# Optimization experiments

Hardware: AMD Instinct MI355X
Metric: run time of the kernel (lower is better)

The kernel has to match this reference:

```python
import jax, jax.numpy as jnp
import numpy as np

EPS = 1e-6
N_HEADS = 8


def causal_dot_product(q, k, v):
    # q,k: [n,h,l,d]; v: [n,h,l,m]
    kv = jnp.einsum('nhld,nhlm->nhldm', k, v)          # [n,h,l,d,m] (large, matches original)
    kv = jnp.cumsum(kv, axis=2)
    return jnp.einsum('nhld,nhldm->nhlm', q, kv)


def flow_attention_causal(queries, keys, values, Wq, bq, Wk, bk, Wv, bv, Wo, bo):
    B, L, _ = queries.shape
    H = N_HEADS
    # projections + split heads -> [B,H,L,Dh]
    def proj(x, W, b):
        y = x @ W + b
        return y.reshape(B, L, H, -1).transpose(0, 2, 1, 3)
    q = jax.nn.sigmoid(proj(queries, Wq, bq))
    k = jax.nn.sigmoid(proj(keys, Wk, bk))
    v = proj(values, Wv, bv)

    normal = (jnp.arange(L, dtype=q.dtype) + 1.0)[None, None, :]  # [1,1,L]

    sink_incoming = 1.0 / jnp.einsum('nhld,nhld->nhl', q + EPS, jnp.cumsum(k, axis=2) + EPS)
    source_outgoing = 1.0 / jnp.einsum('nhld,nhld->nhl', k + EPS, jnp.cumsum(q, axis=2) + EPS)
    sink_incoming = sink_incoming * normal
    source_outgoing = source_outgoing * normal

    conserved_sink = jnp.einsum('nhld,nhld->nhl', q + EPS,
                                jnp.cumsum(k * source_outgoing[..., None], axis=2) + EPS) / normal
    conserved_source = jnp.einsum('nhld,nhld->nhl', k + EPS,
                                  jnp.cumsum(q * sink_incoming[..., None], axis=2) + EPS) / normal
    conserved_source = jnp.clip(conserved_source, -1.0, 1.0)

    sink_allocation = jax.nn.sigmoid(conserved_sink)
    conserved_source = jnp.exp(conserved_source)
    source_competition = conserved_source / jnp.cumsum(conserved_source, axis=-1) * normal

    x = causal_dot_product(q * (sink_incoming / normal)[..., None],
                           k,
                           v * source_competition[..., None]) * sink_allocation[..., None]
    x = x.transpose(0, 2, 1, 3).reshape(B, L, -1)
    return x @ Wo + bo  # dropout is identity at eval


def setup_inputs() -> dict:
    key = jax.random.key(0)
    ks = jax.random.split(key, 11)
    B, L, Din, Dm, Dout = 2, 1024, 512, 512, 512
    s = 0.02
    return {
        'queries': jax.random.normal(ks[0], (B, L, Din), jnp.float32),
        'keys': jax.random.normal(ks[1], (B, L, Din), jnp.float32),
        'values': jax.random.normal(ks[2], (B, L, Din), jnp.float32),
        'Wq': jax.random.normal(ks[3], (Din, Dm), jnp.float32) * s,
        'bq': jnp.zeros((Dm,), jnp.float32),
        'Wk': jax.random.normal(ks[4], (Din, Dm), jnp.float32) * s,
        'bk': jnp.zeros((Dm,), jnp.float32),
        'Wv': jax.random.normal(ks[5], (Din, Dm), jnp.float32) * s,
        'bv': jnp.zeros((Dm,), jnp.float32),
        'Wo': jax.random.normal(ks[6], (Dm, Dout), jnp.float32) * s,
        'bo': jnp.zeros((Dout,), jnp.float32),
    }


def reference(queries, keys, values, Wq, bq, Wk, bk, Wv, bv, Wo, bo):
    return flow_attention_causal(queries, keys, values, Wq, bq, Wk, bk, Wv, bv, Wo, bo)
```

## Files before the change

kernel.cpp:

```cpp
#include <hip/hip_runtime.h>
#include <math.h>

#define EPSF 1e-6f

constexpr int B_  = 2;
constexpr int L_  = 1024;
constexpr int D_  = 512;
constexpr int H_  = 8;
constexpr int DH_ = 64;
constexpr int BL_ = B_ * L_;
constexpr int BH_ = B_ * H_;
constexpr int CT_ = 64;
constexpr int NC_ = L_ / CT_;

typedef __attribute__((ext_vector_type(8))) short bf16x8;
typedef __attribute__((ext_vector_type(4))) float f32x4;

__device__ __forceinline__ unsigned short f2bf(float f) {
  union { float f; unsigned int u; } v; v.f = f;
  const unsigned int u = v.u;
  return (unsigned short)((u + 0x7FFFu + ((u >> 16) & 1u)) >> 16);
}
__device__ __forceinline__ float bf2f(unsigned short u) {
  union { unsigned int u; float f; } v; v.u = ((unsigned int)u) << 16;
  return v.f;
}

__device__ __forceinline__ int sw(int row, int col) {
  return row * 64 + (col ^ ((row & 7) << 3));
}

__global__ __launch_bounds__(256) void proj3_k(const float* __restrict__ Qin,
                                               const float* __restrict__ Kin,
                                               const float* __restrict__ Vin,
                                               const float* __restrict__ Wq,
                                               const float* __restrict__ bq,
                                               const float* __restrict__ Wk,
                                               const float* __restrict__ bk,
                                               const float* __restrict__ Wv,
                                               const float* __restrict__ bv,
                                               unsigned short* __restrict__ Qb,
                                               unsigned short* __restrict__ Kb,
                                               unsigned short* __restrict__ Vb,
                                               float* __restrict__ sumQ,
                                               float* __restrict__ sumK) {
  const int z = blockIdx.z;
  const float* A    = (z == 0) ? Qin : (z == 1) ? Kin : Vin;
  const float* W    = (z == 0) ? Wq  : (z == 1) ? Wk  : Wv;
  const float* bias = (z == 0) ? bq  : (z == 1) ? bk  : bv;
  unsigned short* out = (z == 0) ? Qb : (z == 1) ? Kb : Vb;
  float* csum       = (z == 0) ? sumQ : (z == 1) ? sumK : nullptr;
  const bool sig = (z < 2);

  __shared__ __align__(16) short Als[64 * 40];
  __shared__ __align__(16) short Bls[64 * 40];
  const int tid = threadIdx.x;
  const int m0 = blockIdx.x * 64, n0 = blockIdx.y * 64;
  const int arow = tid >> 2, akq = (tid & 3) << 3;
  const int bcol = tid & 63, bk0 = (tid >> 6) << 3;
  const int lane = tid & 63, wid = tid >> 6;
  const int wr = wid >> 1, wc = wid & 1;
  const int lrow = lane & 15, lk = (lane >> 4) << 3;

  f32x4 acc[2][2] = {{{0.f, 0.f, 0.f, 0.f}, {0.f, 0.f, 0.f, 0.f}},
                     {{0.f, 0.f, 0.f, 0.f}, {0.f, 0.f, 0.f, 0.f}}};
  float ra[8], rb[8];

  auto loadAB = [&](int kt) {
    const float4 f0 = *(const float4*)&A[(size_t)(m0 + arow) * D_ + kt + akq];
    const float4 f1 = *(const float4*)&A[(size_t)(m0 + arow) * D_ + kt + akq + 4];
    ra[0] = f0.x; ra[1] = f0.y; ra[2] = f0.z; ra[3] = f0.w;
    ra[4] = f1.x; ra[5] = f1.y; ra[6] = f1.z; ra[7] = f1.w;
    const float* gw = &W[(size_t)(kt + bk0) * D_ + n0 + bcol];
#pragma unroll
    for (int j = 0; j < 8; ++j) rb[j] = gw[(size_t)j * D_];
  };
  auto writeLDS = [&]() {
    bf16x8 pa, pb;
#pragma unroll
    for (int j = 0; j < 8; ++j) {
      pa[j] = (short)f2bf(ra[j]);
      pb[j] = (short)f2bf(rb[j]);
    }
    *(bf16x8*)&Als[arow * 40 + akq] = pa;
    *(bf16x8*)&Bls[bcol * 40 + bk0] = pb;
  };
  auto compute = [&]() {
    bf16x8 a0 = *(const bf16x8*)&Als[(wr * 32 + lrow) * 40 + lk];
    bf16x8 a1 = *(const bf16x8*)&Als[(wr * 32 + 16 + lrow) * 40 + lk];
    bf16x8 b0 = *(const bf16x8*)&Bls[(wc * 32 + lrow) * 40 + lk];
    bf16x8 b1 = *(const bf16x8*)&Bls[(wc * 32 + 16 + lrow) * 40 + lk];
    acc[0][0] = __builtin_amdgcn_mfma_f32_16x16x32_bf16(a0, b0, acc[0][0], 0, 0, 0);
    acc[0][1] = __builtin_amdgcn_mfma_f32_16x16x32_bf16(a0, b1, acc[0][1], 0, 0, 0);
    acc[1][0] = __builtin_amdgcn_mfma_f32_16x16x32_bf16(a1, b0, acc[1][0], 0, 0, 0);
    acc[1][1] = __builtin_amdgcn_mfma_f32_16x16x32_bf16(a1, b1, acc[1][1], 0, 0, 0);
  };

  loadAB(0);
  writeLDS();
  for (int kt = 32; kt < D_; kt += 32) {
    loadAB(kt);
    __syncthreads();
    compute();
    __syncthreads();
    writeLDS();
  }
  __syncthreads();
  compute();

  const int b = m0 >> 10, h = n0 >> 6;
  float psum[2] = {0.f, 0.f};
#pragma unroll
  for (int j = 0; j < 2; ++j) {
    const int col = n0 + wc * 32 + j * 16 + lrow;
    const float bv4 = bias[col];
    const int dh = col & 63;
#pragma unroll
    for (int i = 0; i < 2; ++i) {
#pragma unroll
      for (int r = 0; r < 4; ++r) {
        const int row = m0 + wr * 32 + i * 16 + (lane >> 4) * 4 + r;
        float x = acc[i][j][r] + bv4;
        if (sig) x = 1.0f / (1.0f + expf(-x));
        const unsigned short ub = f2bf(x);
        const int l = row & (L_ - 1);
        out[(((size_t)(b * H_ + h)) * L_ + l) * DH_ + dh] = ub;
        psum[j] += bf2f(ub);
      }
    }
  }
  if (csum) {
    float* sumS = (float*)Als;
#pragma unroll
    for (int j = 0; j < 2; ++j) {
      psum[j] += __shfl_xor(psum[j], 16);
      psum[j] += __shfl_xor(psum[j], 32);
      if ((lane >> 4) == 0) sumS[wr * 64 + wc * 32 + j * 16 + lrow] = psum[j];
    }
    __syncthreads();
    if (tid < 64) {
      const int c = (m0 & (L_ - 1)) >> 6;
      const int bc = (b * H_ + h) * NC_ + c;
      csum[bc * DH_ + tid] = sumS[tid] + sumS[64 + tid];
    }
  }
}

__global__ __launch_bounds__(256) void flow_phase1_k(const unsigned short* __restrict__ Qb,
                                                     const unsigned short* __restrict__ Kb,
                                                     const float* __restrict__ sumQ,
                                                     const float* __restrict__ sumK,
                                                     float* __restrict__ qscale,
                                                     float* __restrict__ si_a,
                                                     float* __restrict__ so_a,
                                                     float* __restrict__ sumQSI,
                                                     float* __restrict__ sumKSO) {
  const int bc = blockIdx.x, bh = bc >> 4, c = bc & (NC_ - 1);
  const int g = bc * CT_;
  const int tid = threadIdx.x, lane = tid & 63, w = tid >> 6;
  __shared__ float qS[64][65], kS[64][65];
  __shared__ float pqS[64], pkS[64];
  __shared__ float aS[4][64], bS[4][64];
  __shared__ float siS[64], soS[64];
#pragma unroll
  for (int it = 0; it < 2; ++it) {
    const int i8 = it * 256 + tid;
    const int row = i8 >> 3, d0 = (i8 & 7) << 3;
    const bf16x8 qv = *(const bf16x8*)&Qb[(size_t)g * DH_ + i8 * 8];
    const bf16x8 kv = *(const bf16x8*)&Kb[(size_t)g * DH_ + i8 * 8];
#pragma unroll
    for (int j = 0; j < 8; ++j) {
      qS[row][d0 + j] = bf2f((unsigned short)qv[j]);
      kS[row][d0 + j] = bf2f((unsigned short)kv[j]);
    }
  }
  if (tid < 64) {
    float pq = 0.f, pk = 0.f;
    for (int cc = 0; cc < c; ++cc) {
      pq += sumQ[(bh * NC_ + cc) * DH_ + tid];
      pk += sumK[(bh * NC_ + cc) * DH_ + tid];
    }
    pqS[tid] = pq; pkS[tid] = pk;
  }
  __syncthreads();
  float ap = 0.f, bp = 0.f;
  for (int dd = 0; dd < 16; ++dd) {
    const int d = w * 16 + dd;
    const float qv = qS[lane][d];
    const float kv = kS[lane][d];
    float ck = kv, cq = qv;
#pragma unroll
    for (int off = 1; off < 64; off <<= 1) {
      const float t1 = __shfl_up(ck, off);
      const float t2 = __shfl_up(cq, off);
      ck += (lane >= off) ? t1 : 0.f;
      cq += (lane >= off) ? t2 : 0.f;
    }
    ck += pkS[d];
    cq += pqS[d];
    ap += (qv + EPSF) * (ck + EPSF);
    bp += (kv + EPSF) * (cq + EPSF);
  }
  aS[w][lane] = ap; bS[w][lane] = bp;
  __syncthreads();
  const float normal = (float)(c * CT_ + lane + 1);
  if (w == 0) {
    const float a = aS[0][lane] + aS[1][lane] + aS[2][lane] + aS[3][lane];
    const float b = bS[0][lane] + bS[1][lane] + bS[2][lane] + bS[3][lane];
    const float si = normal / a, so = normal / b;
    qscale[g + lane] = 1.0f / a;
    si_a[g + lane] = si;
    so_a[g + lane] = so;
    siS[lane] = si; soS[lane] = so;
  }
  __syncthreads();
  float sq = 0.f, sk = 0.f;
#pragma unroll
  for (int li = 0; li < 16; ++li) {
    const int l = w * 16 + li;
    sq += qS[l][lane] * siS[l];
    sk += kS[l][lane] * soS[l];
  }
  aS[w][lane] = sq; bS[w][lane] = sk;
  __syncthreads();
  if (tid < 64) {
    sumQSI[bc * DH_ + tid] = aS[0][tid] + aS[1][tid] + aS[2][tid] + aS[3][tid];
    sumKSO[bc * DH_ + tid] = bS[0][tid] + bS[1][tid] + bS[2][tid] + bS[3][tid];
  }
}

__global__ __launch_bounds__(256) void flow_phase2_k(const unsigned short* __restrict__ Qb,
                                                     const unsigned short* __restrict__ Kb,
                                                     const float* __restrict__ sumQSI,
                                                     const float* __restrict__ sumKSO,
                                                     const float* __restrict__ si_a,
                                                     const float* __restrict__ so_a,
                                                     float* __restrict__ salloc,
                                                     float* __restrict__ e_a,
                                                     float* __restrict__ sumE) {
  const int bc = blockIdx.x, bh = bc >> 4, c = bc & (NC_ - 1);
  const int g = bc * CT_;
  const int tid = threadIdx.x, lane = tid & 63, w = tid >> 6;
  __shared__ float qS[64][65], kS[64][65];
  __shared__ float pqS[64], pkS[64];
  __shared__ float aS[4][64], bS[4][64];
#pragma unroll
  for (int it = 0; it < 2; ++it) {
    const int i8 = it * 256 + tid;
    const int row = i8 >> 3, d0 = (i8 & 7) << 3;
    const bf16x8 qv = *(const bf16x8*)&Qb[(size_t)g * DH_ + i8 * 8];
    const bf16x8 kv = *(const bf16x8*)&Kb[(size_t)g * DH_ + i8 * 8];
#pragma unroll
    for (int j = 0; j < 8; ++j) {
      qS[row][d0 + j] = bf2f((unsigned short)qv[j]);
      kS[row][d0 + j] = bf2f((unsigned short)kv[j]);
    }
  }
  if (tid < 64) {
    float pq = 0.f, pk = 0.f;
    for (int cc = 0; cc < c; ++cc) {
      pq += sumQSI[(bh * NC_ + cc) * DH_ + tid];
      pk += sumKSO[(bh * NC_ + cc) * DH_ + tid];
    }
    pqS[tid] = pq; pkS[tid] = pk;
  }
  __syncthreads();
  const float si = si_a[g + lane];
  const float so = so_a[g + lane];
  float c1p = 0.f, c2p = 0.f;
  for (int dd = 0; dd < 16; ++dd) {
    const int d = w * 16 + dd;
    const float qv = qS[lane][d];
    const float kv = kS[lane][d];
    float ckso = kv * so, cqsi = qv * si;
#pragma unroll
    for (int off = 1; off < 64; off <<= 1) {
      const float t1 = __shfl_up(ckso, off);
      const float t2 = __shfl_up(cqsi, off);
      ckso += (lane >= off) ? t1 : 0.f;
      cqsi += (lane >= off) ? t2 : 0.f;
    }
    ckso += pkS[d];
    cqsi += pqS[d];
    c1p += (qv + EPSF) * (ckso + EPSF);
    c2p += (kv + EPSF) * (cqsi + EPSF);
  }
  aS[w][lane] = c1p; bS[w][lane] = c2p;
  __syncthreads();
  if (w == 0) {
    const float c1 = aS[0][lane] + aS[1][lane] + aS[2][lane] + aS[3][lane];
    const float c2 = bS[0][lane] + bS[1][lane] + bS[2][lane] + bS[3][lane];
    const float normal = (float)(c * CT_ + lane + 1);
    const float cs_sink = c1 / normal;
    salloc[g + lane] = 1.0f / (1.0f + expf(-cs_sink));
    float cs_src = c2 / normal;
    cs_src = fminf(1.0f, fmaxf(-1.0f, cs_src));
    const float e = expf(cs_src);
    e_a[g + lane] = e;
    float tot = e;
#pragma unroll
    for (int off = 32; off; off >>= 1) tot += __shfl_xor(tot, off);
    if (lane == 0) sumE[bc] = tot;
  }
}

__global__ __launch_bounds__(256) void flow_ckv_k(const unsigned short* __restrict__ K16,
                                                  const unsigned short* __restrict__ V16,
                                                  const float* __restrict__ e_a,
                                                  const float* __restrict__ sumE,
                                                  float* __restrict__ comp,
                                                  float* __restrict__ KV) {
  const int bc = blockIdx.x, bh = bc >> 4, c = bc & (NC_ - 1);
  const int g = bc * CT_;
  const int tid = threadIdx.x;
  __shared__ float compS[CT_];
  __shared__ __align__(16) unsigned short kT16[64 * 64];
  __shared__ __align__(16) unsigned short vT16[64 * 64];
  if (tid < 64) {
    const int lane = tid;
    const float e = e_a[g + lane];
    float se = (lane < c) ? sumE[bh * NC_ + lane] : 0.f;
#pragma unroll
    for (int off = 32; off; off >>= 1) se += __shfl_xor(se, off);
    float s = e;
#pragma unroll
    for (int off = 1; off < 64; off <<= 1) {
      const float t = __shfl_up(s, off);
      s += (lane >= off) ? t : 0.f;
    }
    const float cf = e / (se + s) * (float)(c * CT_ + lane + 1);
    compS[lane] = cf;
    comp[g + lane] = cf;
  }
  __syncthreads();
#pragma unroll
  for (int it = 0; it < 2; ++it) {
    const int i8 = it * 256 + tid;
    const int l = i8 >> 3, d0 = (i8 & 7) << 3;
    const bf16x8 kv = *(const bf16x8*)&K16[(size_t)g * DH_ + i8 * 8];
    const bf16x8 vv = *(const bf16x8*)&V16[(size_t)g * DH_ + i8 * 8];
    const float cl = compS[l];
#pragma unroll
    for (int j = 0; j < 8; ++j) {
      kT16[sw(d0 + j, l)] = (unsigned short)kv[j];
      vT16[sw(d0 + j, l)] = f2bf(bf2f((unsigned short)vv[j]) * cl);
    }
  }
  __syncthreads();
  const int lane = tid & 63, w = tid >> 6;
  const int fr = lane & 15, fk = (lane >> 4) << 3;
  f32x4 acc[4] = {{0.f, 0.f, 0.f, 0.f}, {0.f, 0.f, 0.f, 0.f},
                  {0.f, 0.f, 0.f, 0.f}, {0.f, 0.f, 0.f, 0.f}};
  const bf16x8 a0 = *(const bf16x8*)&kT16[sw(w * 16 + fr, fk)];
  const bf16x8 a1 = *(const bf16x8*)&kT16[sw(w * 16 + fr, fk + 32)];
#pragma unroll
  for (int cb = 0; cb < 4; ++cb) {
    const bf16x8 b0 = *(const bf16x8*)&vT16[sw(cb * 16 + fr, fk)];
    const bf16x8 b1 = *(const bf16x8*)&vT16[sw(cb * 16 + fr, fk + 32)];
    acc[cb] = __builtin_amdgcn_mfma_f32_16x16x32_bf16(a0, b0, acc[cb], 0, 0, 0);
    acc[cb] = __builtin_amdgcn_mfma_f32_16x16x32_bf16(a1, b1, acc[cb], 0, 0, 0);
  }
  float* outp = KV + (size_t)bc * DH_ * DH_;
#pragma unroll
  for (int r = 0; r < 4; ++r) {
    const int d = w * 16 + (lane >> 4) * 4 + r;
#pragma unroll
    for (int cb = 0; cb < 4; ++cb) outp[d * DH_ + cb * 16 + fr] = acc[cb][r];
  }
}

__global__ __launch_bounds__(256) void kv_prefix_k(float* __restrict__ KV) {
  const int idx = blockIdx.x * 256 + threadIdx.x;
  const int bh = idx >> 12, p = idx & 4095;
  const size_t base = (size_t)bh * NC_ * DH_ * DH_ + p;
  float run = 0.f;
#pragma unroll
  for (int c = 0; c < NC_; ++c) {
    const float t = KV[base + (size_t)c * DH_ * DH_];
    KV[base + (size_t)c * DH_ * DH_] = run;
    run += t;
  }
}

__global__ __launch_bounds__(256) void attn_k(const unsigned short* __restrict__ Q16,
                                              const unsigned short* __restrict__ K16,
                                              const unsigned short* __restrict__ V16,
                                              const float* __restrict__ KVp,
                                              const float* __restrict__ qscale,
                                              const float* __restrict__ salloc,
                                              const float* __restrict__ comp,
                                              unsigned short* __restrict__ X) {
  const int bc = blockIdx.x;
  const int bh = bc >> 4, c = bc & (NC_ - 1);
  const int bb = bh >> 3, hh = bh & (H_ - 1);
  const int g = bc * CT_;
  __shared__ __align__(16) unsigned short qp16[64 * 64];
  __shared__ __align__(16) unsigned short k16[64 * 64];
  __shared__ __align__(16) unsigned short vT16[64 * 64];
  __shared__ __align__(16) unsigned short kvT16[64 * 64];
  __shared__ __align__(16) unsigned short S16[64 * 64];
  const int tid = threadIdx.x;
#pragma unroll
  for (int it = 0; it < 2; ++it) {
    const int i8 = it * 256 + tid;
    const int r = i8 >> 3, d0 = (i8 & 7) << 3;
    const bf16x8 qv = *(const bf16x8*)&Q16[(size_t)g * DH_ + i8 * 8];
    const bf16x8 kv = *(const bf16x8*)&K16[(size_t)g * DH_ + i8 * 8];
    const bf16x8 vv = *(const bf16x8*)&V16[(size_t)g * DH_ + i8 * 8];
    const float qs = qscale[g + r];
    const float cl = comp[g + r];
    bf16x8 pq;
#pragma unroll
    for (int j = 0; j < 8; ++j) pq[j] = (short)f2bf(bf2f((unsigned short)qv[j]) * qs);
    *(bf16x8*)&qp16[sw(r, d0)] = pq;
    *(bf16x8*)&k16[sw(r, d0)] = kv;
#pragma unroll
    for (int j = 0; j < 8; ++j)
      vT16[sw(d0 + j, r)] = f2bf(bf2f((unsigned short)vv[j]) * cl);
  }
  for (int i4 = tid; i4 < DH_ * DH_ / 4; i4 += 256) {
    const int d = i4 >> 4, m0 = (i4 & 15) << 2;
    const float4 t = *(const float4*)&KVp[(size_t)bc * DH_ * DH_ + d * DH_ + m0];
    kvT16[sw(m0 + 0, d)] = f2bf(t.x);
    kvT16[sw(m0 + 1, d)] = f2bf(t.y);
    kvT16[sw(m0 + 2, d)] = f2bf(t.z);
    kvT16[sw(m0 + 3, d)] = f2bf(t.w);
  }
  __syncthreads();

  const int lane = tid & 63, w = tid >> 6;
  const int fr = lane & 15, fk = (lane >> 4) << 3;
  const int arow = w * 16 + fr;
  f32x4 accX[4] = {{0.f, 0.f, 0.f, 0.f}, {0.f, 0.f, 0.f, 0.f},
                   {0.f, 0.f, 0.f, 0.f}, {0.f, 0.f, 0.f, 0.f}};
  f32x4 accS[4] = {{0.f, 0.f, 0.f, 0.f}, {0.f, 0.f, 0.f, 0.f},
                   {0.f, 0.f, 0.f, 0.f}, {0.f, 0.f, 0.f, 0.f}};

  const bf16x8 aq0 = *(const bf16x8*)&qp16[sw(arow, fk)];
  const bf16x8 aq1 = *(const bf16x8*)&qp16[sw(arow, fk + 32)];
#pragma unroll
  for (int cb = 0; cb < 4; ++cb) {
    const int bcol = cb * 16 + fr;
    const bf16x8 bv0 = *(const bf16x8*)&kvT16[sw(bcol, fk)];
    const bf16x8 bv1 = *(const bf16x8*)&kvT16[sw(bcol, fk + 32)];
    accX[cb] = __builtin_amdgcn_mfma_f32_16x16x32_bf16(aq0, bv0, accX[cb], 0, 0, 0);
    accX[cb] = __builtin_amdgcn_mfma_f32_16x16x32_bf16(aq1, bv1, accX[cb], 0, 0, 0);
    const bf16x8 bk0 = *(const bf16x8*)&k16[sw(bcol, fk)];
    const bf16x8 bk1 = *(const bf16x8*)&k16[sw(bcol, fk + 32)];
    accS[cb] = __builtin_amdgcn_mfma_f32_16x16x32_bf16(aq0, bk0, accS[cb], 0, 0, 0);
    accS[cb] = __builtin_amdgcn_mfma_f32_16x16x32_bf16(aq1, bk1, accS[cb], 0, 0, 0);
  }
#pragma unroll
  for (int cb = 0; cb < 4; ++cb) {
#pragma unroll
    for (int r = 0; r < 4; ++r) {
      const int l = w * 16 + (lane >> 4) * 4 + r;
      const int j = cb * 16 + fr;
      S16[sw(l, j)] = (j <= l) ? f2bf(accS[cb][r]) : (unsigned short)0;
    }
  }
  __syncthreads();
  const bf16x8 as0 = *(const bf16x8*)&S16[sw(arow, fk)];
  const bf16x8 as1 = *(const bf16x8*)&S16[sw(arow, fk + 32)];
#pragma unroll
  for (int cb = 0; cb < 4; ++cb) {
    const int bcol = cb * 16 + fr;
    const bf16x8 bv0 = *(const bf16x8*)&vT16[sw(bcol, fk)];
    const bf16x8 bv1 = *(const bf16x8*)&vT16[sw(bcol, fk + 32)];
    accX[cb] = __builtin_amdgcn_mfma_f32_16x16x32_bf16(as0, bv0, accX[cb], 0, 0, 0);
    accX[cb] = __builtin_amdgcn_mfma_f32_16x16x32_bf16(as1, bv1, accX[cb], 0, 0, 0);
  }
#pragma unroll
  for (int r = 0; r < 4; ++r) {
    const int l = w * 16 + (lane >> 4) * 4 + r;
    const float sal = salloc[g + l];
    const size_t rowbase = ((size_t)(bb * L_ + c * CT_ + l)) * D_ + hh * DH_;
#pragma unroll
    for (int cb = 0; cb < 4; ++cb) {
      const int m = cb * 16 + fr;
      X[rowbase + m] = f2bf(accX[cb][r] * sal);
    }
  }
}

__global__ __launch_bounds__(256) void gemm_out_k(const unsigned short* __restrict__ A,
                                                  const float* __restrict__ W,
                                                  const float* __restrict__ bias,
                                                  float* __restrict__ out) {
  __shared__ __align__(16) short Als[64 * 40];
  __shared__ __align__(16) short Bls[64 * 40];
  const int tid = threadIdx.x;
  const int m0 = blockIdx.x * 64, n0 = blockIdx.y * 64;
  const int arow = tid >> 2, akq = (tid & 3) << 3;
  const int bcol = tid & 63, bk0 = (tid >> 6) << 3;
  const int lane = tid & 63, wid = tid >> 6;
  const int wr = wid >> 1, wc = wid & 1;
  const int lrow = lane & 15, lk = (lane >> 4) << 3;

  f32x4 acc[2][2] = {{{0.f, 0.f, 0.f, 0.f}, {0.f, 0.f, 0.f, 0.f}},
                     {{0.f, 0.f, 0.f, 0.f}, {0.f, 0.f, 0.f, 0.f}}};
  bf16x8 pa;
  float rb[8];
  auto loadAB = [&](int kt) {
    pa = *(const bf16x8*)&A[(size_t)(m0 + arow) * D_ + kt + akq];
    const float* gw = &W[(size_t)(kt + bk0) * D_ + n0 + bcol];
#pragma unroll
    for (int j = 0; j < 8; ++j) rb[j] = gw[(size_t)j * D_];
  };
  auto writeLDS = [&]() {
    bf16x8 pb;
#pragma unroll
    for (int j = 0; j < 8; ++j) pb[j] = (short)f2bf(rb[j]);
    *(bf16x8*)&Als[arow * 40 + akq] = pa;
    *(bf16x8*)&Bls[bcol * 40 + bk0] = pb;
  };
  auto compute = [&]() {
    bf16x8 a0 = *(const bf16x8*)&Als[(wr * 32 + lrow) * 40 + lk];
    bf16x8 a1 = *(const bf16x8*)&Als[(wr * 32 + 16 + lrow) * 40 + lk];
    bf16x8 b0 = *(const bf16x8*)&Bls[(wc * 32 + lrow) * 40 + lk];
    bf16x8 b1 = *(const bf16x8*)&Bls[(wc * 32 + 16 + lrow) * 40 + lk];
    acc[0][0] = __builtin_amdgcn_mfma_f32_16x16x32_bf16(a0, b0, acc[0][0], 0, 0, 0);
    acc[0][1] = __builtin_amdgcn_mfma_f32_16x16x32_bf16(a0, b1, acc[0][1], 0, 0, 0);
    acc[1][0] = __builtin_amdgcn_mfma_f32_16x16x32_bf16(a1, b0, acc[1][0], 0, 0, 0);
    acc[1][1] = __builtin_amdgcn_mfma_f32_16x16x32_bf16(a1, b1, acc[1][1], 0, 0, 0);
  };

  loadAB(0);
  writeLDS();
  for (int kt = 32; kt < D_; kt += 32) {
    loadAB(kt);
    __syncthreads();
    compute();
    __syncthreads();
    writeLDS();
  }
  __syncthreads();
  compute();

#pragma unroll
  for (int j = 0; j < 2; ++j) {
    const int col = n0 + wc * 32 + j * 16 + lrow;
    const float bv4 = bias[col];
#pragma unroll
    for (int i = 0; i < 2; ++i) {
#pragma unroll
      for (int r = 0; r < 4; ++r) {
        const int row = m0 + wr * 32 + i * 16 + (lane >> 4) * 4 + r;
        out[(size_t)row * D_ + col] = acc[i][j][r] + bv4;
      }
    }
  }
}

extern "C" void kernel_launch(void* const* d_in, const int* in_sizes, int n_in,
                              void* d_out, int out_size, void* d_ws, size_t ws_size,
                              hipStream_t stream) {
  (void)in_sizes; (void)n_in; (void)out_size; (void)ws_size;
  const float* queries = (const float*)d_in[0];
  const float* keys    = (const float*)d_in[1];
  const float* values  = (const float*)d_in[2];
  const float* Wq = (const float*)d_in[3];
  const float* bq = (const float*)d_in[4];
  const float* Wk = (const float*)d_in[5];
  const float* bk = (const float*)d_in[6];
  const float* Wv = (const float*)d_in[7];
  const float* bv = (const float*)d_in[8];
  const float* Wo = (const float*)d_in[9];
  const float* bo = (const float*)d_in[10];

  const size_t seg = (size_t)BH_ * L_ * DH_;
  unsigned short* Qb = (unsigned short*)d_ws;
  unsigned short* Kb = Qb + seg;
  unsigned short* Vb = Kb + seg;
  float* KVb = (float*)(Vb + seg);
  float* p   = KVb + (size_t)BH_ * NC_ * DH_ * DH_;
  float* qscale = p; p += BH_ * L_;
  float* salloc = p; p += BH_ * L_;
  float* comp   = p; p += BH_ * L_;
  float* si_a   = p; p += BH_ * L_;
  float* so_a   = p; p += BH_ * L_;
  float* e_a    = p; p += BH_ * L_;
  float* sumQ   = p; p += BH_ * NC_ * DH_;
  float* sumK   = p; p += BH_ * NC_ * DH_;
  float* sumQSI = p; p += BH_ * NC_ * DH_;
  float* sumKSO = p; p += BH_ * NC_ * DH_;
  float* sumE   = p; p += BH_ * NC_;
  unsigned short* Xb16 = (unsigned short*)p;

  proj3_k<<<dim3(BL_ / 64, D_ / 64, 3), 256, 0, stream>>>(
      queries, keys, values, Wq, bq, Wk, bk, Wv, bv, Qb, Kb, Vb, sumQ, sumK);
  flow_phase1_k<<<BH_ * NC_, 256, 0, stream>>>(Qb, Kb, sumQ, sumK,
                                               qscale, si_a, so_a, sumQSI, sumKSO);
  flow_phase2_k<<<BH_ * NC_, 256, 0, stream>>>(Qb, Kb, sumQSI, sumKSO, si_a, so_a,
                                               salloc, e_a, sumE);
  flow_ckv_k<<<BH_ * NC_, 256, 0, stream>>>(Kb, Vb, e_a, sumE, comp, KVb);
  kv_prefix_k<<<BH_ * NC_, 256, 0, stream>>>(KVb);
  attn_k<<<BH_ * NC_, 256, 0, stream>>>(Qb, Kb, Vb, KVb, qscale, salloc, comp, Xb16);
  gemm_out_k<<<dim3(BL_ / 64, D_ / 64), 256, 0, stream>>>(Xb16, Wo, bo, (float*)d_out);
}
```

Measured before the change: 62.66 us.

## Pre-transpose weights to bf16 and fold KV prefix scan into attention

Adds a kernel that converts and transposes all four weight matrices to bf16 once per call, so the projection and output GEMMs load B tiles with contiguous 16-byte reads instead of eight strided fp32 loads plus conversion. It also removes the separate KV prefix-scan kernel; each attention block now sums all preceding chunk KV matrices itself with a masked loop over every chunk. This saves one launch and one read-write pass, but multiplies KV reads in the attention kernel, since each block reads all 16 chunks of its head.

```diff
diff --git a/kernel.cpp b/kernel.cpp
--- a/kernel.cpp
+++ b/kernel.cpp
@@ -30,14 +30,38 @@
   return row * 64 + (col ^ ((row & 7) << 3));
 }
 
+__global__ __launch_bounds__(256) void convw_k(const float* __restrict__ Wq,
+                                               const float* __restrict__ Wk,
+                                               const float* __restrict__ Wv,
+                                               const float* __restrict__ Wo,
+                                               unsigned short* __restrict__ WT) {
+  const int z = blockIdx.z;
+  const float* W = (z == 0) ? Wq : (z == 1) ? Wk : (z == 2) ? Wv : Wo;
+  unsigned short* O = WT + (size_t)z * D_ * D_;
+  __shared__ float t[64][65];
+  const int tid = threadIdx.x;
+  const int k0 = blockIdx.x * 64, n0 = blockIdx.y * 64;
+#pragma unroll
+  for (int it = 0; it < 16; ++it) {
+    const int idx = it * 256 + tid;
+    const int r = idx >> 6, c = idx & 63;
+    t[r][c] = W[(size_t)(k0 + r) * D_ + n0 + c];
+  }
+  __syncthreads();
+#pragma unroll
+  for (int it = 0; it < 16; ++it) {
+    const int idx = it * 256 + tid;
+    const int r = idx >> 6, c = idx & 63;
+    O[(size_t)(n0 + r) * D_ + k0 + c] = f2bf(t[c][r]);
+  }
+}
+
 __global__ __launch_bounds__(256) void proj3_k(const float* __restrict__ Qin,
                                                const float* __restrict__ Kin,
                                                const float* __restrict__ Vin,
-                                               const float* __restrict__ Wq,
+                                               const unsigned short* __restrict__ WT,
                                                const float* __restrict__ bq,
-                                               const float* __restrict__ Wk,
                                                const float* __restrict__ bk,
-                                               const float* __restrict__ Wv,
                                                const float* __restrict__ bv,
                                                unsigned short* __restrict__ Qb,
                                                unsigned short* __restrict__ Kb,
@@ -46,7 +70,7 @@
                                                float* __restrict__ sumK) {
   const int z = blockIdx.z;
   const float* A    = (z == 0) ? Qin : (z == 1) ? Kin : Vin;
-  const float* W    = (z == 0) ? Wq  : (z == 1) ? Wk  : Wv;
+  const unsigned short* Wt = WT + (size_t)z * D_ * D_;
   const float* bias = (z == 0) ? bq  : (z == 1) ? bk  : bv;
   unsigned short* out = (z == 0) ? Qb : (z == 1) ? Kb : Vb;
   float* csum       = (z == 0) ? sumQ : (z == 1) ? sumK : nullptr;
@@ -57,33 +81,28 @@
   const int tid = threadIdx.x;
   const int m0 = blockIdx.x * 64, n0 = blockIdx.y * 64;
   const int arow = tid >> 2, akq = (tid & 3) << 3;
-  const int bcol = tid & 63, bk0 = (tid >> 6) << 3;
   const int lane = tid & 63, wid = tid >> 6;
   const int wr = wid >> 1, wc = wid & 1;
   const int lrow = lane & 15, lk = (lane >> 4) << 3;
 
   f32x4 acc[2][2] = {{{0.f, 0.f, 0.f, 0.f}, {0.f, 0.f, 0.f, 0.f}},
                      {{0.f, 0.f, 0.f, 0.f}, {0.f, 0.f, 0.f, 0.f}}};
-  float ra[8], rb[8];
+  float ra[8];
+  bf16x8 pb;
 
   auto loadAB = [&](int kt) {
     const float4 f0 = *(const float4*)&A[(size_t)(m0 + arow) * D_ + kt + akq];
     const float4 f1 = *(const float4*)&A[(size_t)(m0 + arow) * D_ + kt + akq + 4];
     ra[0] = f0.x; ra[1] = f0.y; ra[2] = f0.z; ra[3] = f0.w;
     ra[4] = f1.x; ra[5] = f1.y; ra[6] = f1.z; ra[7] = f1.w;
-    const float* gw = &W[(size_t)(kt + bk0) * D_ + n0 + bcol];
-#pragma unroll
-    for (int j = 0; j < 8; ++j) rb[j] = gw[(size_t)j * D_];
+    pb = *(const bf16x8*)&Wt[(size_t)(n0 + arow) * D_ + kt + akq];
   };
   auto writeLDS = [&]() {
-    bf16x8 pa, pb;
-#pragma unroll
-    for (int j = 0; j < 8; ++j) {
-      pa[j] = (short)f2bf(ra[j]);
-      pb[j] = (short)f2bf(rb[j]);
-    }
+    bf16x8 pa;
+#pragma unroll
+    for (int j = 0; j < 8; ++j) pa[j] = (short)f2bf(ra[j]);
     *(bf16x8*)&Als[arow * 40 + akq] = pa;
-    *(bf16x8*)&Bls[bcol * 40 + bk0] = pb;
+    *(bf16x8*)&Bls[arow * 40 + akq] = pb;
   };
   auto compute = [&]() {
     bf16x8 a0 = *(const bf16x8*)&Als[(wr * 32 + lrow) * 40 + lk];
@@ -369,23 +388,10 @@
   }
 }
 
-__global__ __launch_bounds__(256) void kv_prefix_k(float* __restrict__ KV) {
-  const int idx = blockIdx.x * 256 + threadIdx.x;
-  const int bh = idx >> 12, p = idx & 4095;
-  const size_t base = (size_t)bh * NC_ * DH_ * DH_ + p;
-  float run = 0.f;
-#pragma unroll
-  for (int c = 0; c < NC_; ++c) {
-    const float t = KV[base + (size_t)c * DH_ * DH_];
-    KV[base + (size_t)c * DH_ * DH_] = run;
-    run += t;
-  }
-}
-
 __global__ __launch_bounds__(256) void attn_k(const unsigned short* __restrict__ Q16,
                                               const unsigned short* __restrict__ K16,
                                               const unsigned short* __restrict__ V16,
-                                              const float* __restrict__ KVp,
+                                              const float* __restrict__ KVraw,
                                               const float* __restrict__ qscale,
                                               const float* __restrict__ salloc,
                                               const float* __restrict__ comp,
@@ -418,13 +424,22 @@
     for (int j = 0; j < 8; ++j)
       vT16[sw(d0 + j, r)] = f2bf(bf2f((unsigned short)vv[j]) * cl);
   }
-  for (int i4 = tid; i4 < DH_ * DH_ / 4; i4 += 256) {
-    const int d = i4 >> 4, m0 = (i4 & 15) << 2;
-    const float4 t = *(const float4*)&KVp[(size_t)bc * DH_ * DH_ + d * DH_ + m0];
-    kvT16[sw(m0 + 0, d)] = f2bf(t.x);
-    kvT16[sw(m0 + 1, d)] = f2bf(t.y);
-    kvT16[sw(m0 + 2, d)] = f2bf(t.z);
-    kvT16[sw(m0 + 3, d)] = f2bf(t.w);
+  {
+    const float* kvbh = KVraw + (size_t)bh * NC_ * DH_ * DH_;
+    for (int i4 = tid; i4 < DH_ * DH_ / 4; i4 += 256) {
+      const int d = i4 >> 4, mg = (i4 & 15) << 2;
+      float s0 = 0.f, s1 = 0.f, s2 = 0.f, s3 = 0.f;
+#pragma unroll
+      for (int cc = 0; cc < NC_; ++cc) {
+        const float4 t = *(const float4*)&kvbh[(size_t)cc * (DH_ * DH_) + d * DH_ + mg];
+        const float msk = (cc < c) ? 1.f : 0.f;
+        s0 += t.x * msk; s1 += t.y * msk; s2 += t.z * msk; s3 += t.w * msk;
+      }
+      kvT16[sw(mg + 0, d)] = f2bf(s0);
+      kvT16[sw(mg + 1, d)] = f2bf(s1);
+      kvT16[sw(mg + 2, d)] = f2bf(s2);
+      kvT16[sw(mg + 3, d)] = f2bf(s3);
+    }
   }
   __syncthreads();
 
@@ -484,7 +499,7 @@
 }
 
 __global__ __launch_bounds__(256) void gemm_out_k(const unsigned short* __restrict__ A,
-                                                  const float* __restrict__ W,
+                                                  const unsigned short* __restrict__ WoT,
                                                   const float* __restrict__ bias,
                                                   float* __restrict__ out) {
   __shared__ __align__(16) short Als[64 * 40];
@@ -492,27 +507,20 @@
   const int tid = threadIdx.x;
   const int m0 = blockIdx.x * 64, n0 = blockIdx.y * 64;
   const int arow = tid >> 2, akq = (tid & 3) << 3;
-  const int bcol = tid & 63, bk0 = (tid >> 6) << 3;
   const int lane = tid & 63, wid = tid >> 6;
   const int wr = wid >> 1, wc = wid & 1;
   const int lrow = lane & 15, lk = (lane >> 4) << 3;
 
   f32x4 acc[2][2] = {{{0.f, 0.f, 0.f, 0.f}, {0.f, 0.f, 0.f, 0.f}},
                      {{0.f, 0.f, 0.f, 0.f}, {0.f, 0.f, 0.f, 0.f}}};
-  bf16x8 pa;
-  float rb[8];
+  bf16x8 pa, pb;
   auto loadAB = [&](int kt) {
     pa = *(const bf16x8*)&A[(size_t)(m0 + arow) * D_ + kt + akq];
-    const float* gw = &W[(size_t)(kt + bk0) * D_ + n0 + bcol];
-#pragma unroll
-    for (int j = 0; j < 8; ++j) rb[j] = gw[(size_t)j * D_];
+    pb = *(const bf16x8*)&WoT[(size_t)(n0 + arow) * D_ + kt + akq];
   };
   auto writeLDS = [&]() {
-    bf16x8 pb;
-#pragma unroll
-    for (int j = 0; j < 8; ++j) pb[j] = (short)f2bf(rb[j]);
     *(bf16x8*)&Als[arow * 40 + akq] = pa;
-    *(bf16x8*)&Bls[bcol * 40 + bk0] = pb;
+    *(bf16x8*)&Bls[arow * 40 + akq] = pb;
   };
   auto compute = [&]() {
     bf16x8 a0 = *(const bf16x8*)&Als[(wr * 32 + lrow) * 40 + lk];
@@ -572,7 +580,9 @@
   unsigned short* Qb = (unsigned short*)d_ws;
   unsigned short* Kb = Qb + seg;
   unsigned short* Vb = Kb + seg;
-  float* KVb = (float*)(Vb + seg);
+  unsigned short* WT = Vb + seg;
+  unsigned short* Xb16 = WT + (size_t)4 * D_ * D_;
+  float* KVb = (float*)(Xb16 + (size_t)BL_ * D_);
   float* p   = KVb + (size_t)BH_ * NC_ * DH_ * DH_;
   float* qscale = p; p += BH_ * L_;
   float* salloc = p; p += BH_ * L_;
@@ -585,16 +595,16 @@
   float* sumQSI = p; p += BH_ * NC_ * DH_;
   float* sumKSO = p; p += BH_ * NC_ * DH_;
   float* sumE   = p; p += BH_ * NC_;
-  unsigned short* Xb16 = (unsigned short*)p;
-
+
+  convw_k<<<dim3(8, 8, 4), 256, 0, stream>>>(Wq, Wk, Wv, Wo, WT);
   proj3_k<<<dim3(BL_ / 64, D_ / 64, 3), 256, 0, stream>>>(
-      queries, keys, values, Wq, bq, Wk, bk, Wv, bv, Qb, Kb, Vb, sumQ, sumK);
+      queries, keys, values, WT, bq, bk, bv, Qb, Kb, Vb, sumQ, sumK);
   flow_phase1_k<<<BH_ * NC_, 256, 0, stream>>>(Qb, Kb, sumQ, sumK,
                                                qscale, si_a, so_a, sumQSI, sumKSO);
   flow_phase2_k<<<BH_ * NC_, 256, 0, stream>>>(Qb, Kb, sumQSI, sumKSO, si_a, so_a,
                                                salloc, e_a, sumE);
   flow_ckv_k<<<BH_ * NC_, 256, 0, stream>>>(Kb, Vb, e_a, sumE, comp, KVb);
-  kv_prefix_k<<<BH_ * NC_, 256, 0, stream>>>(KVb);
   attn_k<<<BH_ * NC_, 256, 0, stream>>>(Qb, Kb, Vb, KVb, qscale, salloc, comp, Xb16);
-  gemm_out_k<<<dim3(BL_ / 64, D_ / 64), 256, 0, stream>>>(Xb16, Wo, bo, (float*)d_out);
-}
+  gemm_out_k<<<dim3(BL_ / 64, D_ / 64), 256, 0, stream>>>(
+      Xb16, WT + (size_t)3 * D_ * D_, bo, (float*)d_out);
+}
```

Measured after the change: 65.35 us. 4.3% more time.

## Fuse KV chunk prefix into attention kernel and double GEMM K-tile to 64

Applied to the files above, without the earlier changes.

Removes the separate kv_prefix_k launch: each attention block now sums all preceding chunk KV states itself, masking out chunks at or after its own index, while reading every chunk. This saves one kernel launch and its read/write pass over the KV buffer, at the cost of redundant loads that grow with chunk count (16 chunks, each a 64x64 float tile per block). Separately, both projection GEMMs now use a K-tile of 64 instead of 32, halving the number of barrier-separated iterations but increasing register and LDS use.

```diff
diff --git a/kernel.cpp b/kernel.cpp
--- a/kernel.cpp
+++ b/kernel.cpp
@@ -52,53 +52,62 @@
   float* csum       = (z == 0) ? sumQ : (z == 1) ? sumK : nullptr;
   const bool sig = (z < 2);
 
-  __shared__ __align__(16) short Als[64 * 40];
-  __shared__ __align__(16) short Bls[64 * 40];
+  __shared__ __align__(16) short Als[64 * 72];
+  __shared__ __align__(16) short Bls[64 * 72];
   const int tid = threadIdx.x;
   const int m0 = blockIdx.x * 64, n0 = blockIdx.y * 64;
-  const int arow = tid >> 2, akq = (tid & 3) << 3;
-  const int bcol = tid & 63, bk0 = (tid >> 6) << 3;
+  const int arow = tid >> 2, ak0 = (tid & 3) << 4;
+  const int bcol = tid & 63, bk0 = (tid >> 6) << 4;
   const int lane = tid & 63, wid = tid >> 6;
   const int wr = wid >> 1, wc = wid & 1;
   const int lrow = lane & 15, lk = (lane >> 4) << 3;
 
   f32x4 acc[2][2] = {{{0.f, 0.f, 0.f, 0.f}, {0.f, 0.f, 0.f, 0.f}},
                      {{0.f, 0.f, 0.f, 0.f}, {0.f, 0.f, 0.f, 0.f}}};
-  float ra[8], rb[8];
+  float ra[16], rb[16];
 
   auto loadAB = [&](int kt) {
-    const float4 f0 = *(const float4*)&A[(size_t)(m0 + arow) * D_ + kt + akq];
-    const float4 f1 = *(const float4*)&A[(size_t)(m0 + arow) * D_ + kt + akq + 4];
-    ra[0] = f0.x; ra[1] = f0.y; ra[2] = f0.z; ra[3] = f0.w;
-    ra[4] = f1.x; ra[5] = f1.y; ra[6] = f1.z; ra[7] = f1.w;
+#pragma unroll
+    for (int j = 0; j < 4; ++j) {
+      const float4 f = *(const float4*)&A[(size_t)(m0 + arow) * D_ + kt + ak0 + 4 * j];
+      ra[4 * j + 0] = f.x; ra[4 * j + 1] = f.y; ra[4 * j + 2] = f.z; ra[4 * j + 3] = f.w;
+    }
     const float* gw = &W[(size_t)(kt + bk0) * D_ + n0 + bcol];
 #pragma unroll
-    for (int j = 0; j < 8; ++j) rb[j] = gw[(size_t)j * D_];
+    for (int j = 0; j < 16; ++j) rb[j] = gw[(size_t)j * D_];
   };
   auto writeLDS = [&]() {
-    bf16x8 pa, pb;
+    bf16x8 pa0, pa1, pb0, pb1;
 #pragma unroll
     for (int j = 0; j < 8; ++j) {
-      pa[j] = (short)f2bf(ra[j]);
-      pb[j] = (short)f2bf(rb[j]);
-    }
-    *(bf16x8*)&Als[arow * 40 + akq] = pa;
-    *(bf16x8*)&Bls[bcol * 40 + bk0] = pb;
+      pa0[j] = (short)f2bf(ra[j]);
+      pa1[j] = (short)f2bf(ra[j + 8]);
+      pb0[j] = (short)f2bf(rb[j]);
+      pb1[j] = (short)f2bf(rb[j + 8]);
+    }
+    *(bf16x8*)&Als[arow * 72 + ak0] = pa0;
+    *(bf16x8*)&Als[arow * 72 + ak0 + 8] = pa1;
+    *(bf16x8*)&Bls[bcol * 72 + bk0] = pb0;
+    *(bf16x8*)&Bls[bcol * 72 + bk0 + 8] = pb1;
   };
   auto compute = [&]() {
-    bf16x8 a0 = *(const bf16x8*)&Als[(wr * 32 + lrow) * 40 + lk];
-    bf16x8 a1 = *(const bf16x8*)&Als[(wr * 32 + 16 + lrow) * 40 + lk];
-    bf16x8 b0 = *(const bf16x8*)&Bls[(wc * 32 + lrow) * 40 + lk];
-    bf16x8 b1 = *(const bf16x8*)&Bls[(wc * 32 + 16 + lrow) * 40 + lk];
-    acc[0][0] = __builtin_amdgcn_mfma_f32_16x16x32_bf16(a0, b0, acc[0][0], 0, 0, 0);
-    acc[0][1] = __builtin_amdgcn_mfma_f32_16x16x32_bf16(a0, b1, acc[0][1], 0, 0, 0);
-    acc[1][0] = __builtin_amdgcn_mfma_f32_16x16x32_bf16(a1, b0, acc[1][0], 0, 0, 0);
-    acc[1][1] = __builtin_amdgcn_mfma_f32_16x16x32_bf16(a1, b1, acc[1][1], 0, 0, 0);
+#pragma unroll
+    for (int ks = 0; ks < 2; ++ks) {
+      const int ko = ks * 32 + lk;
+      bf16x8 a0 = *(const bf16x8*)&Als[(wr * 32 + lrow) * 72 + ko];
+      bf16x8 a1 = *(const bf16x8*)&Als[(wr * 32 + 16 + lrow) * 72 + ko];
+      bf16x8 b0 = *(const bf16x8*)&Bls[(wc * 32 + lrow) * 72 + ko];
+      bf16x8 b1 = *(const bf16x8*)&Bls[(wc * 32 + 16 + lrow) * 72 + ko];
+      acc[0][0] = __builtin_amdgcn_mfma_f32_16x16x32_bf16(a0, b0, acc[0][0], 0, 0, 0);
+      acc[0][1] = __builtin_amdgcn_mfma_f32_16x16x32_bf16(a0, b1, acc[0][1], 0, 0, 0);
+      acc[1][0] = __builtin_amdgcn_mfma_f32_16x16x32_bf16(a1, b0, acc[1][0], 0, 0, 0);
+      acc[1][1] = __builtin_amdgcn_mfma_f32_16x16x32_bf16(a1, b1, acc[1][1], 0, 0, 0);
+    }
   };
 
   loadAB(0);
   writeLDS();
-  for (int kt = 32; kt < D_; kt += 32) {
+  for (int kt = 64; kt < D_; kt += 64) {
     loadAB(kt);
     __syncthreads();
     compute();
@@ -369,23 +378,10 @@
   }
 }
 
-__global__ __launch_bounds__(256) void kv_prefix_k(float* __restrict__ KV) {
-  const int idx = blockIdx.x * 256 + threadIdx.x;
-  const int bh = idx >> 12, p = idx & 4095;
-  const size_t base = (size_t)bh * NC_ * DH_ * DH_ + p;
-  float run = 0.f;
-#pragma unroll
-  for (int c = 0; c < NC_; ++c) {
-    const float t = KV[base + (size_t)c * DH_ * DH_];
-    KV[base + (size_t)c * DH_ * DH_] = run;
-    run += t;
-  }
-}
-
 __global__ __launch_bounds__(256) void attn_k(const unsigned short* __restrict__ Q16,
                                               const unsigned short* __restrict__ K16,
                                               const unsigned short* __restrict__ V16,
-                                              const float* __restrict__ KVp,
+                                              const float* __restrict__ KVraw,
                                               const float* __restrict__ qscale,
                                               const float* __restrict__ salloc,
                                               const float* __restrict__ comp,
@@ -418,13 +414,22 @@
     for (int j = 0; j < 8; ++j)
       vT16[sw(d0 + j, r)] = f2bf(bf2f((unsigned short)vv[j]) * cl);
   }
-  for (int i4 = tid; i4 < DH_ * DH_ / 4; i4 += 256) {
-    const int d = i4 >> 4, m0 = (i4 & 15) << 2;
-    const float4 t = *(const float4*)&KVp[(size_t)bc * DH_ * DH_ + d * DH_ + m0];
-    kvT16[sw(m0 + 0, d)] = f2bf(t.x);
-    kvT16[sw(m0 + 1, d)] = f2bf(t.y);
-    kvT16[sw(m0 + 2, d)] = f2bf(t.z);
-    kvT16[sw(m0 + 3, d)] = f2bf(t.w);
+  {
+    const float* kvbh = KVraw + (size_t)bh * NC_ * DH_ * DH_;
+    for (int i4 = tid; i4 < DH_ * DH_ / 4; i4 += 256) {
+      const int d = i4 >> 4, mg = (i4 & 15) << 2;
+      float s0 = 0.f, s1 = 0.f, s2 = 0.f, s3 = 0.f;
+#pragma unroll
+      for (int cc = 0; cc < NC_; ++cc) {
+        const float4 t = *(const float4*)&kvbh[(size_t)cc * (DH_ * DH_) + d * DH_ + mg];
+        const float msk = (cc < c) ? 1.f : 0.f;
+        s0 += t.x * msk; s1 += t.y * msk; s2 += t.z * msk; s3 += t.w * msk;
+      }
+      kvT16[sw(mg + 0, d)] = f2bf(s0);
+      kvT16[sw(mg + 1, d)] = f2bf(s1);
+      kvT16[sw(mg + 2, d)] = f2bf(s2);
+      kvT16[sw(mg + 3, d)] = f2bf(s3);
+    }
   }
   __syncthreads();
 
@@ -487,47 +492,57 @@
                                                   const float* __restrict__ W,
                                                   const float* __restrict__ bias,
                                                   float* __restrict__ out) {
-  __shared__ __align__(16) short Als[64 * 40];
-  __shared__ __align__(16) short Bls[64 * 40];
+  __shared__ __align__(16) short Als[64 * 72];
+  __shared__ __align__(16) short Bls[64 * 72];
   const int tid = threadIdx.x;
   const int m0 = blockIdx.x * 64, n0 = blockIdx.y * 64;
-  const int arow = tid >> 2, akq = (tid & 3) << 3;
-  const int bcol = tid & 63, bk0 = (tid >> 6) << 3;
+  const int arow = tid >> 2, ak0 = (tid & 3) << 4;
+  const int bcol = tid & 63, bk0 = (tid >> 6) << 4;
   const int lane = tid & 63, wid = tid >> 6;
   const int wr = wid >> 1, wc = wid & 1;
   const int lrow = lane & 15, lk = (lane >> 4) << 3;
 
   f32x4 acc[2][2] = {{{0.f, 0.f, 0.f, 0.f}, {0.f, 0.f, 0.f, 0.f}},
                      {{0.f, 0.f, 0.f, 0.f}, {0.f, 0.f, 0.f, 0.f}}};
-  bf16x8 pa;
-  float rb[8];
+  bf16x8 pa0, pa1;
+  float rb[16];
   auto loadAB = [&](int kt) {
-    pa = *(const bf16x8*)&A[(size_t)(m0 + arow) * D_ + kt + akq];
+    pa0 = *(const bf16x8*)&A[(size_t)(m0 + arow) * D_ + kt + ak0];
+    pa1 = *(const bf16x8*)&A[(size_t)(m0 + arow) * D_ + kt + ak0 + 8];
     const float* gw = &W[(size_t)(kt + bk0) * D_ + n0 + bcol];
 #pragma unroll
-    for (int j = 0; j < 8; ++j) rb[j] = gw[(size_t)j * D_];
+    for (int j = 0; j < 16; ++j) rb[j] = gw[(size_t)j * D_];
   };
   auto writeLDS = [&]() {
-    bf16x8 pb;
-#pragma unroll
-    for (int j = 0; j < 8; ++j) pb[j] = (short)f2bf(rb[j]);
-    *(bf16x8*)&Als[arow * 40 + akq] = pa;
-    *(bf16x8*)&Bls[bcol * 40 + bk0] = pb;
+    bf16x8 pb0, pb1;
+#pragma unroll
+    for (int j = 0; j < 8; ++j) {
+      pb0[j] = (short)f2bf(rb[j]);
+      pb1[j] = (short)f2bf(rb[j + 8]);
+    }
+    *(bf16x8*)&Als[arow * 72 + ak0] = pa0;
+    *(bf16x8*)&Als[arow * 72 + ak0 + 8] = pa1;
+    *(bf16x8*)&Bls[bcol * 72 + bk0] = pb0;
+    *(bf16x8*)&Bls[bcol * 72 + bk0 + 8] = pb1;
   };
   auto compute = [&]() {
-    bf16x8 a0 = *(const bf16x8*)&Als[(wr * 32 + lrow) * 40 + lk];
-    bf16x8 a1 = *(const bf16x8*)&Als[(wr * 32 + 16 + lrow) * 40 + lk];
-    bf16x8 b0 = *(const bf16x8*)&Bls[(wc * 32 + lrow) * 40 + lk];
-    bf16x8 b1 = *(const bf16x8*)&Bls[(wc * 32 + 16 + lrow) * 40 + lk];
-    acc[0][0] = __builtin_amdgcn_mfma_f32_16x16x32_bf16(a0, b0, acc[0][0], 0, 0, 0);
-    acc[0][1] = __builtin_amdgcn_mfma_f32_16x16x32_bf16(a0, b1, acc[0][1], 0, 0, 0);
-    acc[1][0] = __builtin_amdgcn_mfma_f32_16x16x32_bf16(a1, b0, acc[1][0], 0, 0, 0);
-    acc[1][1] = __builtin_amdgcn_mfma_f32_16x16x32_bf16(a1, b1, acc[1][1], 0, 0, 0);
+#pragma unroll
+    for (int ks = 0; ks < 2; ++ks) {
+      const int ko = ks * 32 + lk;
+      bf16x8 a0 = *(const bf16x8*)&Als[(wr * 32 + lrow) * 72 + ko];
+      bf16x8 a1 = *(const bf16x8*)&Als[(wr * 32 + 16 + lrow) * 72 + ko];
+      bf16x8 b0 = *(const bf16x8*)&Bls[(wc * 32 + lrow) * 72 + ko];
+      bf16x8 b1 = *(const bf16x8*)&Bls[(wc * 32 + 16 + lrow) * 72 + ko];
+      acc[0][0] = __builtin_amdgcn_mfma_f32_16x16x32_bf16(a0, b0, acc[0][0], 0, 0, 0);
+      acc[0][1] = __builtin_amdgcn_mfma_f32_16x16x32_bf16(a0, b1, acc[0][1], 0, 0, 0);
+      acc[1][0] = __builtin_amdgcn_mfma_f32_16x16x32_bf16(a1, b0, acc[1][0], 0, 0, 0);
+      acc[1][1] = __builtin_amdgcn_mfma_f32_16x16x32_bf16(a1, b1, acc[1][1], 0, 0, 0);
+    }
   };
 
   loadAB(0);
   writeLDS();
-  for (int kt = 32; kt < D_; kt += 32) {
+  for (int kt = 64; kt < D_; kt += 64) {
     loadAB(kt);
     __syncthreads();
     compute();
@@ -594,7 +609,6 @@
   flow_phase2_k<<<BH_ * NC_, 256, 0, stream>>>(Qb, Kb, sumQSI, sumKSO, si_a, so_a,
                                                salloc, e_a, sumE);
   flow_ckv_k<<<BH_ * NC_, 256, 0, stream>>>(Kb, Vb, e_a, sumE, comp, KVb);
-  kv_prefix_k<<<BH_ * NC_, 256, 0, stream>>>(KVb);
   attn_k<<<BH_ * NC_, 256, 0, stream>>>(Qb, Kb, Vb, KVb, qscale, salloc, comp, Xb16);
   gemm_out_k<<<dim3(BL_ / 64, D_ / 64), 256, 0, stream>>>(Xb16, Wo, bo, (float*)d_out);
 }
```

New measurement: 63.45 us. Within noise of the previous version (+1.3%).
